# Kernel optimization log

Measured on AMD Instinct MI355X. Metric: run time of the kernel, lower is better.

The kernel has to match this reference:

```python
import jax, jax.numpy as jnp
import numpy as np

EPS = 1e-5

def conv2d(x, w, b=None, pad=0, groups=1):
    # x: NCHW, w: OIHW
    y = jax.lax.conv_general_dilated(
        x, w, window_strides=(1, 1), padding=[(pad, pad), (pad, pad)],
        dimension_numbers=('NCHW', 'OIHW', 'NCHW'), feature_group_count=groups)
    if b is not None:
        y = y + b[None, :, None, None]
    return y

def layernorm_c(x, w, b):
    # WithBias LayerNorm over channel dim of NCHW (matches to_3d -> LN(last dim=c) -> to_4d)
    mu = jnp.mean(x, axis=1, keepdims=True)
    var = jnp.mean((x - mu) ** 2, axis=1, keepdims=True)
    return (x - mu) / jnp.sqrt(var + EPS) * w[None, :, None, None] + b[None, :, None, None]

def setup_inputs() -> dict:
    key = jax.random.key(0)
    ks = iter(jax.random.split(key, 40))
    C, C8, Cc, Cs = 64, 8, 21, 2  # dim, dim//8, dim//compress_ratio, dim//squeeze_factor
    H = W = 64
    B = 4
    Hm = 128  # mlp hidden = dim * mlp_ratio
    s = 0.05
    def rn(shape):
        return jax.random.normal(next(ks), shape, dtype=jnp.float32) * s
    return {
        'x': jax.random.normal(next(ks), (B, C, H, W), dtype=jnp.float32),
        'ln_w': jnp.ones((C,), jnp.float32),
        'ln_b': jnp.zeros((C,), jnp.float32),
        'sab_q_w': rn((C8, C, 1, 1)), 'sab_q_b': rn((C8,)),
        'sab_k_w': rn((C8, C, 1, 1)), 'sab_k_b': rn((C8,)),
        'sab_v_w': rn((C, C, 1, 1)), 'sab_v_b': rn((C,)),
        'sab_qkdw_w': rn((C8, 1, 3, 3)), 'sab_qkdw_b': rn((C8,)),
        'sab_vdw_w': rn((C, 1, 3, 3)), 'sab_vdw_b': rn((C,)),
        'sab_proj_w': rn((C, C, 1, 1)), 'sab_proj_b': rn((C,)),
        'sab_gamma': jnp.zeros((1,), jnp.float32) + 0.1,
        'cab_w1': rn((Cc, C, 3, 3)), 'cab_b1': rn((Cc,)),
        'cab_w2': rn((C, Cc, 3, 3)), 'cab_b2': rn((C,)),
        'ca_w1': rn((Cs, C, 1, 1)), 'ca_b1': rn((Cs,)),
        'ca_w2': rn((C, Cs, 1, 1)), 'ca_b2': rn((C,)),
        'fc1_w': rn((Hm, C)), 'fc1_b': rn((Hm,)),
        'fc2_w': rn((C, Hm)), 'fc2_b': rn((C,)),
    }

def reference(x, ln_w, ln_b,
              sab_q_w, sab_q_b, sab_k_w, sab_k_b, sab_v_w, sab_v_b,
              sab_qkdw_w, sab_qkdw_b, sab_vdw_w, sab_vdw_b,
              sab_proj_w, sab_proj_b, sab_gamma,
              cab_w1, cab_b1, cab_w2, cab_b2,
              ca_w1, ca_b1, ca_w2, ca_b2,
              fc1_w, fc1_b, fc2_w, fc2_b):
    b, c, h, w = x.shape
    hw = h * w
    shortcut = x
    xn = layernorm_c(x, ln_w, ln_b)

    # --- SAB: full-pixel spatial self-attention ---
    C8 = sab_q_w.shape[0]
    q = conv2d(conv2d(xn, sab_q_w, sab_q_b), sab_qkdw_w, sab_qkdw_b, pad=1, groups=C8)
    k = conv2d(conv2d(xn, sab_k_w, sab_k_b), sab_qkdw_w, sab_qkdw_b, pad=1, groups=C8)
    v = conv2d(conv2d(xn, sab_v_w, sab_v_b), sab_vdw_w, sab_vdw_b, pad=1, groups=c)
    qf = q.reshape(b, C8, hw)          # (b, c8, n)
    kf = k.reshape(b, C8, hw)
    vf = v.reshape(b, c, hw)
    energy = jnp.einsum('bdi,bdj->bij', qf, kf)      # (b, hw, hw)
    attn = jax.nn.softmax(energy, axis=-1)
    out = jnp.einsum('bcj,bij->bci', vf, attn)        # (b, c, hw)
    out = out.reshape(b, c, h, w)
    out = conv2d(out, sab_proj_w, sab_proj_b)
    sa_feat = sab_gamma[0] * out + xn

    # --- CAB: conv compress/expand + RCAN channel attention ---
    y = conv2d(xn, cab_w1, cab_b1, pad=1)
    y = jax.nn.gelu(y, approximate=False)
    y = conv2d(y, cab_w2, cab_b2, pad=1)
    p = jnp.mean(y, axis=(2, 3), keepdims=True)       # adaptive avg pool to 1x1
    p = jax.nn.relu(conv2d(p, ca_w1, ca_b1))
    p = jax.nn.sigmoid(conv2d(p, ca_w2, ca_b2))
    ca_feat = y * p

    feat_sum = sa_feat + ca_feat + shortcut

    # --- MLP over channels (note: output is reshaped, NOT permuted back — faithful to source) ---
    fs1 = layernorm_c(feat_sum, ln_w, ln_b)
    t = fs1.transpose(0, 2, 3, 1).reshape(b, hw, c)   # (b, hw, c)
    t = jax.nn.gelu(t @ fc1_w.T + fc1_b, approximate=False)
    t = t @ fc2_w.T + fc2_b
    feat_sum2 = t.reshape(b, c, h, w)                 # raw view, matching torch .view(b,c,h,w)
    return feat_sum2 + feat_sum
```

## Files before the change

kernel.cpp:

```cpp
#include <hip/hip_runtime.h>
#include <math.h>

#define NB 4
#define NC 64
#define NC8 8
#define NCC 21
#define NHW 4096
#define NHM 128

typedef __attribute__((ext_vector_type(8))) short bf16x8;
typedef __attribute__((ext_vector_type(8))) unsigned short ushort8;
typedef __attribute__((ext_vector_type(4))) float f32x4;

__device__ __forceinline__ float gelu_exact(float x) {
    return 0.5f * x * (1.0f + erff(x * 0.70710678118654752f));
}

__device__ __forceinline__ unsigned short f2bf(float x) {
    union { float f; unsigned u; } u; u.f = x;
    unsigned r = u.u + 0x7fffu + ((u.u >> 16) & 1u);
    return (unsigned short)(r >> 16);
}

__device__ __forceinline__ float bf2f(unsigned short v) {
    union { unsigned u; float f; } t; t.u = (unsigned)v << 16; return t.f;
}

__global__ __launch_bounds__(256) void k_prep(const float* __restrict__ qw, const float* __restrict__ kw,
                     const float* __restrict__ vw, const float* __restrict__ c1w,
                     const float* __restrict__ c2w, const float* __restrict__ pw,
                     const float* __restrict__ f1w, const float* __restrict__ f2w,
                     float* __restrict__ o, float* __restrict__ pool,
                     const float* __restrict__ x, const float* __restrict__ lnw,
                     const float* __restrict__ lnb,
                     unsigned short* __restrict__ xn, unsigned short* __restrict__ xnT) {
    int bid = blockIdx.x;
    int tid = threadIdx.x;
    if (bid < 244) {
        int idx = bid * 256 + tid;
        if (idx < 256) pool[idx] = 0.f;
        if (idx < 5120) {
            int ci = idx / 80, j = idx - ci * 80;
            float v = j < 8 ? qw[j * 64 + ci] : (j < 16 ? kw[(j - 8) * 64 + ci] : vw[(j - 16) * 64 + ci]);
            o[idx] = v;
        } else if (idx < 9216) {
            int r = idx - 5120; int co = r & 63, ci = r >> 6;
            o[idx] = pw[co * 64 + ci];
        } else if (idx < 27648) {
            int r = idx - 9216;
            int j = r & 7, l = (r >> 3) & 63, s = (r >> 9) % 18, f = r / 9216;
            int co = f * 16 + (l & 15);
            int k = s * 32 + (l >> 4) * 8 + j;
            int tap = k >> 6, ci = k & 63;
            float v = (co < 21) ? c1w[co * 576 + ci * 9 + tap] : 0.f;
            unsigned short hi = f2bf(v);
            unsigned short lo = f2bf(v - bf2f(hi));
            ((unsigned short*)(o + 9216))[r] = hi;
            ((unsigned short*)(o + 18432))[r] = lo;
        } else if (idx < 46080) {
            int r = idx - 27648;
            int j = r & 7, l = (r >> 3) & 63, s = (r >> 9) % 9, f = r / 4608;
            int co = f * 16 + (l & 15);
            int ci = (l >> 4) * 8 + j;
            float v = (ci < 21) ? c2w[co * 189 + ci * 9 + s] : 0.f;
            unsigned short hi = f2bf(v);
            unsigned short lo = f2bf(v - bf2f(hi));
            ((unsigned short*)(o + 27648))[r] = hi;
            ((unsigned short*)(o + 36864))[r] = lo;
        } else if (idx < 54272) {
            int r = idx - 46080;
            int j = r & 7, l = (r >> 3) & 63, q = r >> 9;
            int F = q >> 1, s = q & 1;
            int m = F * 16 + (l & 15);
            int k = s * 32 + (l >> 4) * 8 + j;
            float v = f1w[m * 64 + k];
            unsigned short hi = f2bf(v);
            unsigned short lo = f2bf(v - bf2f(hi));
            ((unsigned short*)(o + 46080))[r] = hi;
            ((unsigned short*)(o + 50176))[r] = lo;
        } else if (idx < 62464) {
            int r = idx - 54272;
            int j = r & 7, l = (r >> 3) & 63, q = r >> 9;
            int F2 = q >> 2, s = q & 3;
            int wo = F2 * 16 + (l & 15);
            int k = s * 32 + (l >> 4) * 8 + j;
            float v = f2w[wo * 128 + k];
            unsigned short hi = f2bf(v);
            unsigned short lo = f2bf(v - bf2f(hi));
            ((unsigned short*)(o + 54272))[r] = hi;
            ((unsigned short*)(o + 58368))[r] = lo;
        }
        return;
    }
    __shared__ float r1[4][64], r2[4][64];
    int lb = bid - 244;
    int pl = tid & 63, cq = tid >> 6;
    int b = lb >> 6;
    int pix = (lb & 63) * 64 + pl;
    const float* p = x + (size_t)b * NC * NHW + pix;
    float v[16]; float s = 0.f, ss = 0.f;
    #pragma unroll
    for (int k = 0; k < 16; ++k) {
        float f = p[(size_t)(cq * 16 + k) * NHW];
        v[k] = f; s += f; ss += f * f;
    }
    r1[cq][pl] = s; r2[cq][pl] = ss;
    __syncthreads();
    float S  = r1[0][pl] + r1[1][pl] + r1[2][pl] + r1[3][pl];
    float SS = r2[0][pl] + r2[1][pl] + r2[2][pl] + r2[3][pl];
    float mean = S * (1.0f / 64);
    float rstd = rsqrtf(SS * (1.0f / 64) - mean * mean + 1e-5f);
    unsigned short* q = xn + (size_t)b * NC * NHW + pix;
    ushort8 t0, t1;
    #pragma unroll
    for (int k = 0; k < 16; ++k) {
        int c = cq * 16 + k;
        unsigned short bv = f2bf((v[k] - mean) * rstd * lnw[c] + lnb[c]);
        q[(size_t)c * NHW] = bv;
        if (k < 8) t0[k] = bv; else t1[k - 8] = bv;
    }
    unsigned short* tp = xnT + ((size_t)b * NHW + pix) * 64 + cq * 16;
    *(ushort8*)tp = t0;
    *(ushort8*)(tp + 8) = t1;
}

__global__ __launch_bounds__(512) void k_qkv(const unsigned short* __restrict__ xn,
        const float* __restrict__ wt, const float* __restrict__ qb,
        const float* __restrict__ kb, const float* __restrict__ vb,
        unsigned short* __restrict__ q1, unsigned short* __restrict__ k1,
        unsigned short* __restrict__ v1) {
    __shared__ unsigned short Xs[64][64];
    __shared__ float Ws[64][80];
    int tid = threadIdx.x;
    int pix0 = blockIdx.x * 64, b = blockIdx.y;
    for (int i = tid; i < 1024; i += 512) {
        int c = i >> 4, q4 = i & 15;
        *(ushort4*)&Xs[c][q4 * 4] = *(const ushort4*)(xn + ((size_t)b * NC + c) * NHW + pix0 + q4 * 4);
    }
    for (int i = tid; i < 1280; i += 512)
        *(float4*)&((float*)Ws)[i * 4] = *(const float4*)&wt[i * 4];
    __syncthreads();
    int p2 = (tid & 31) * 2, g = tid >> 5;
    int co0 = g * 5;
    float a0[5], a1[5];
    #pragma unroll
    for (int j = 0; j < 5; ++j) { a0[j] = 0.f; a1[j] = 0.f; }
    for (int ci = 0; ci < 64; ++ci) {
        ushort2 uv = *(const ushort2*)&Xs[ci][p2];
        float fx = bf2f(uv.x), fy = bf2f(uv.y);
        #pragma unroll
        for (int j = 0; j < 5; ++j) {
            float wv = Ws[ci][co0 + j];
            a0[j] = fmaf(fx, wv, a0[j]);
            a1[j] = fmaf(fy, wv, a1[j]);
        }
    }
    #pragma unroll
    for (int j = 0; j < 5; ++j) {
        int co = co0 + j;
        float bsv; unsigned short* dst;
        if (co < 8)       { bsv = qb[co];      dst = q1 + ((size_t)b * NC8 + co) * NHW + pix0 + p2; }
        else if (co < 16) { bsv = kb[co - 8];  dst = k1 + ((size_t)b * NC8 + co - 8) * NHW + pix0 + p2; }
        else              { bsv = vb[co - 16]; dst = v1 + ((size_t)b * NC + co - 16) * NHW + pix0 + p2; }
        ushort2 o = { f2bf(a0[j] + bsv), f2bf(a1[j] + bsv) };
        *(ushort2*)dst = o;
    }
}

__global__ __launch_bounds__(512) void k_dwcab1(
        const unsigned short* __restrict__ q1, const unsigned short* __restrict__ k1,
        const unsigned short* __restrict__ v1,
        const float* __restrict__ qkw, const float* __restrict__ qkb,
        const float* __restrict__ vw, const float* __restrict__ vb,
        unsigned short* __restrict__ qdb, unsigned short* __restrict__ kdb,
        unsigned short* __restrict__ v8,
        const unsigned short* __restrict__ xnT,
        const unsigned short* __restrict__ Ah, const unsigned short* __restrict__ Al,
        const float* __restrict__ bias, unsigned short* __restrict__ y1T) {
    __shared__ float Rs[2048];
    int bid = blockIdx.x;
    int tid = threadIdx.x;
    if (bid < 2560) {
        int pix = (bid & 7) * 512 + tid;
        int rest = bid >> 3;
        int yv = rest % 80, b = rest / 80;
        int y = pix >> 6, x = pix & 63;
        if (yv < 16) {
            int c = yv & 7;
            const unsigned short* ip = (yv < 8 ? q1 : k1) + ((size_t)b * NC8 + c) * NHW;
            const float* wp = qkw + c * 9;
            float acc = qkb[c];
            #pragma unroll
            for (int dy = -1; dy <= 1; ++dy) {
                int yy = y + dy; if (yy < 0 || yy > 63) continue;
                #pragma unroll
                for (int dx = -1; dx <= 1; ++dx) {
                    int xx = x + dx; if (xx < 0 || xx > 63) continue;
                    acc += wp[(dy + 1) * 3 + (dx + 1)] * bf2f(ip[yy * 64 + xx]);
                }
            }
            (yv < 8 ? qdb : kdb)[((size_t)b * NHW + pix) * NC8 + c] = f2bf(acc);
        } else {
            int c = yv - 16;
            const unsigned short* ip = v1 + ((size_t)b * NC + c) * NHW;
            const float* wp = vw + c * 9;
            float acc = vb[c];
            #pragma unroll
            for (int dy = -1; dy <= 1; ++dy) {
                int yy = y + dy; if (yy < 0 || yy > 63) continue;
                #pragma unroll
                for (int dx = -1; dx <= 1; ++dx) {
                    int xx = x + dx; if (xx < 0 || xx > 63) continue;
                    acc += wp[(dy + 1) * 3 + (dx + 1)] * bf2f(ip[yy * 64 + xx]);
                }
            }
            v8[(((size_t)b * 512 + (pix >> 3)) * NC + c) * 8 + (pix & 7)] = f2bf(acc);
        }
        return;
    }
    int r = bid - 2560;
    int y = r & 63, b = r >> 6;
    int w = tid >> 6, lane = tid & 63;
    int il = lane & 15, g = lane >> 4;
    int frag = w & 3, kh = w >> 2;
    int xloc = frag * 16 + il;
    f32x4 acc[2];
    acc[0] = (f32x4){0.f, 0.f, 0.f, 0.f};
    acc[1] = (f32x4){0.f, 0.f, 0.f, 0.f};
    #pragma unroll
    for (int si = 0; si < 9; ++si) {
        int s = kh * 9 + si;
        int tap = s >> 1;
        int ci0 = (s & 1) * 32;
        int dyv = tap / 3 - 1, dxv = tap - (tap / 3) * 3 - 1;
        int xx = xloc + dxv, yy = y + dyv;
        bf16x8 bv = (bf16x8)(short)0;
        if (((unsigned)xx < 64u) && ((unsigned)yy < 64u))
            bv = *(const bf16x8*)(xnT + ((size_t)b * NHW + yy * 64 + xx) * 64 + ci0 + g * 8);
        #pragma unroll
        for (int f = 0; f < 2; ++f) {
            bf16x8 ahv = *(const bf16x8*)(Ah + ((size_t)(f * 18 + s) * 64 + lane) * 8);
            bf16x8 alv = *(const bf16x8*)(Al + ((size_t)(f * 18 + s) * 64 + lane) * 8);
            acc[f] = __builtin_amdgcn_mfma_f32_16x16x32_bf16(ahv, bv, acc[f], 0, 0, 0);
            acc[f] = __builtin_amdgcn_mfma_f32_16x16x32_bf16(alv, bv, acc[f], 0, 0, 0);
        }
    }
    if (kh == 1) {
        #pragma unroll
        for (int f = 0; f < 2; ++f)
            #pragma unroll
            for (int e = 0; e < 4; ++e)
                Rs[((frag * 2 + f) * 4 + e) * 64 + lane] = acc[f][e];
    }
    __syncthreads();
    if (kh == 0) {
        #pragma unroll
        for (int f = 0; f < 2; ++f) {
            ushort4 pk;
            #pragma unroll
            for (int e = 0; e < 4; ++e) {
                float v = acc[f][e] + Rs[((frag * 2 + f) * 4 + e) * 64 + lane];
                int co = f * 16 + g * 4 + e;
                float rr = 0.f;
                if (co < 21) rr = gelu_exact(v + bias[co]);
                ((unsigned short*)&pk)[e] = f2bf(rr);
            }
            *(ushort4*)(y1T + ((size_t)b * NHW + y * 64 + xloc) * 32 + f * 16 + g * 4) = pk;
        }
    }
}

__global__ __launch_bounds__(512) void k_flashcab2(
        const unsigned short* __restrict__ qdb, const unsigned short* __restrict__ kdb,
        const unsigned short* __restrict__ v8, unsigned short* __restrict__ O,
        const unsigned short* __restrict__ y1T,
        const unsigned short* __restrict__ Ah, const unsigned short* __restrict__ Al,
        const float* __restrict__ bias, unsigned short* __restrict__ ycT,
        float* __restrict__ pool) {
    __shared__ __align__(16) char smem[35840];
    int bid = blockIdx.x;
    int tid = threadIdx.x;
    int w = tid >> 6, lane = tid & 63;
    int g = lane >> 4, il = lane & 15;
    if (bid < 512) {
        int i0 = (bid & 127) * 32, b = bid >> 7;
        unsigned short (*P)[72] = (unsigned short (*)[72])(smem + w * 2304);
        bf16x8 qb0 = (bf16x8)(short)0, qb1 = (bf16x8)(short)0;
        if (g == 0) {
            qb0 = *(const bf16x8*)(qdb + (size_t)(b * NHW + i0 + il) * NC8);
            qb1 = *(const bf16x8*)(qdb + (size_t)(b * NHW + i0 + 16 + il) * NC8);
        }
        f32x4 acc0[4], acc1[4];
        #pragma unroll
        for (int ct = 0; ct < 4; ++ct) {
            acc0[ct] = (f32x4){0.f, 0.f, 0.f, 0.f};
            acc1[ct] = (f32x4){0.f, 0.f, 0.f, 0.f};
        }
        float La0 = 0.f, La1 = 0.f;
        bf16x8 kn[4];
        #pragma unroll
        for (int t = 0; t < 4; ++t) {
            kn[t] = (bf16x8)(short)0;
            if (g == 0) kn[t] = *(const bf16x8*)(kdb + (size_t)(b * NHW + w * 512 + 16 * t + il) * NC8);
        }
        for (int jt = 0; jt < 8; ++jt) {
            int j0 = w * 512 + jt * 64;
            int ch0 = b * 512 + (j0 >> 3);
            bf16x8 va[2][4];
            #pragma unroll
            for (int kc = 0; kc < 2; ++kc)
                #pragma unroll
                for (int ct = 0; ct < 4; ++ct)
                    va[kc][ct] = *(const bf16x8*)(v8 +
                        ((size_t)(ch0 + kc * 4 + g) * NC + ct * 16 + il) * 8);
            bf16x8 ka[4];
            #pragma unroll
            for (int t = 0; t < 4; ++t) ka[t] = kn[t];
            if (jt < 7) {
                #pragma unroll
                for (int t = 0; t < 4; ++t) {
                    kn[t] = (bf16x8)(short)0;
                    if (g == 0) kn[t] = *(const bf16x8*)(kdb + (size_t)(b * NHW + j0 + 64 + 16 * t + il) * NC8);
                }
            }
            #pragma unroll
            for (int t = 0; t < 4; ++t) {
                f32x4 sv = __builtin_amdgcn_mfma_f32_16x16x32_bf16(ka[t], qb0, (f32x4){0.f, 0.f, 0.f, 0.f}, 0, 0, 0);
                float p0 = __expf(sv[0]), p1 = __expf(sv[1]);
                float p2 = __expf(sv[2]), p3 = __expf(sv[3]);
                La0 += (p0 + p1) + (p2 + p3);
                ushort4 pk;
                pk.x = f2bf(p0); pk.y = f2bf(p1); pk.z = f2bf(p2); pk.w = f2bf(p3);
                *(ushort4*)&P[il][16 * t + 4 * g] = pk;
            }
            #pragma unroll
            for (int kc = 0; kc < 2; ++kc) {
                bf16x8 pb = *(const bf16x8*)&P[il][kc * 32 + 8 * g];
                #pragma unroll
                for (int ct = 0; ct < 4; ++ct)
                    acc0[ct] = __builtin_amdgcn_mfma_f32_16x16x32_bf16(va[kc][ct], pb, acc0[ct], 0, 0, 0);
            }
            #pragma unroll
            for (int t = 0; t < 4; ++t) {
                f32x4 sv = __builtin_amdgcn_mfma_f32_16x16x32_bf16(ka[t], qb1, (f32x4){0.f, 0.f, 0.f, 0.f}, 0, 0, 0);
                float p0 = __expf(sv[0]), p1 = __expf(sv[1]);
                float p2 = __expf(sv[2]), p3 = __expf(sv[3]);
                La1 += (p0 + p1) + (p2 + p3);
                ushort4 pk;
                pk.x = f2bf(p0); pk.y = f2bf(p1); pk.z = f2bf(p2); pk.w = f2bf(p3);
                *(ushort4*)&P[il][16 * t + 4 * g] = pk;
            }
            #pragma unroll
            for (int kc = 0; kc < 2; ++kc) {
                bf16x8 pb = *(const bf16x8*)&P[il][kc * 32 + 8 * g];
                #pragma unroll
                for (int ct = 0; ct < 4; ++ct)
                    acc1[ct] = __builtin_amdgcn_mfma_f32_16x16x32_bf16(va[kc][ct], pb, acc1[ct], 0, 0, 0);
            }
        }
        La0 += __shfl_xor(La0, 16, 64); La0 += __shfl_xor(La0, 32, 64);
        La1 += __shfl_xor(La1, 16, 64); La1 += __shfl_xor(La1, 32, 64);

        __syncthreads();
        unsigned short* Ocm = (unsigned short*)smem;
        float* Lw = (float*)(smem + 34816);
        #pragma unroll
        for (int ct = 0; ct < 4; ++ct)
            #pragma unroll
            for (int e = 0; e < 4; ++e) {
                int c = ct * 16 + 4 * g + e;
                Ocm[(w * 2 + 0) * 1088 + c * 17 + il] = f2bf(acc0[ct][e]);
                Ocm[(w * 2 + 1) * 1088 + c * 17 + il] = f2bf(acc1[ct][e]);
            }
        if (lane < 16) {
            Lw[(w * 2 + 0) * 16 + il] = La0;
            Lw[(w * 2 + 1) * 16 + il] = La1;
        }
        __syncthreads();

        int st = tid >> 8, rem = tid & 255;
        int ic = rem & 15, ch = rem >> 4;
        float l = 0.f;
        #pragma unroll
        for (int w2 = 0; w2 < 8; ++w2) l += Lw[(w2 * 2 + st) * 16 + ic];
        float rl = 1.0f / l;
        #pragma unroll
        for (int cc = 0; cc < 4; ++cc) {
            int c = cc * 16 + ch;
            float o = 0.f;
            #pragma unroll
            for (int w2 = 0; w2 < 8; ++w2) o += bf2f(Ocm[(w2 * 2 + st) * 1088 + c * 17 + ic]);
            O[(size_t)(b * NC + c) * NHW + i0 + st * 16 + ic] = f2bf(o * rl);
        }
        return;
    }
    float* Rs = (float*)smem;
    float (*Ssum)[64] = (float (*)[64])(smem + 16384);
    int r = bid - 512;
    int y = r & 63, b = r >> 6;
    int frag = w & 3, kh = w >> 2;
    int xloc = frag * 16 + il;
    f32x4 acc[4];
    #pragma unroll
    for (int f = 0; f < 4; ++f) acc[f] = (f32x4){0.f, 0.f, 0.f, 0.f};
    #pragma unroll
    for (int si = 0; si < 5; ++si) {
        if (!(kh == 1 && si == 4)) {
            int s = kh * 5 + si;
            int dyv = s / 3 - 1, dxv = s - (s / 3) * 3 - 1;
            int xx = xloc + dxv, yy = y + dyv;
            bf16x8 bv = (bf16x8)(short)0;
            if (((unsigned)xx < 64u) && ((unsigned)yy < 64u))
                bv = *(const bf16x8*)(y1T + ((size_t)b * NHW + yy * 64 + xx) * 32 + g * 8);
            #pragma unroll
            for (int f = 0; f < 4; ++f) {
                bf16x8 ahv = *(const bf16x8*)(Ah + ((size_t)(f * 9 + s) * 64 + lane) * 8);
                bf16x8 alv = *(const bf16x8*)(Al + ((size_t)(f * 9 + s) * 64 + lane) * 8);
                acc[f] = __builtin_amdgcn_mfma_f32_16x16x32_bf16(ahv, bv, acc[f], 0, 0, 0);
                acc[f] = __builtin_amdgcn_mfma_f32_16x16x32_bf16(alv, bv, acc[f], 0, 0, 0);
            }
        }
    }
    if (kh == 1) {
        #pragma unroll
        for (int f = 0; f < 4; ++f)
            #pragma unroll
            for (int e = 0; e < 4; ++e)
                Rs[((frag * 4 + f) * 4 + e) * 64 + lane] = acc[f][e];
    }
    __syncthreads();
    if (kh == 0) {
        #pragma unroll
        for (int f = 0; f < 4; ++f) {
            ushort4 pk;
            #pragma unroll
            for (int e = 0; e < 4; ++e) {
                int co = f * 16 + g * 4 + e;
                float v = acc[f][e] + Rs[((frag * 4 + f) * 4 + e) * 64 + lane] + bias[co];
                ((unsigned short*)&pk)[e] = f2bf(v);
                float ps = v;
                ps += __shfl_xor(ps, 1, 64);
                ps += __shfl_xor(ps, 2, 64);
                ps += __shfl_xor(ps, 4, 64);
                ps += __shfl_xor(ps, 8, 64);
                if (il == 0) Ssum[frag][co] = ps;
            }
            *(ushort4*)(ycT + ((size_t)b * NHW + y * 64 + xloc) * 64 + f * 16 + g * 4) = pk;
        }
    }
    __syncthreads();
    if (tid < 64) {
        float t = Ssum[0][tid] + Ssum[1][tid] + Ssum[2][tid] + Ssum[3][tid];
        atomicAdd(&pool[b * NC + tid], t);
    }
}

__global__ __launch_bounds__(512) void k_fsum2(const unsigned short* __restrict__ O,
        const float* __restrict__ pwt, const float* __restrict__ pb,
        const float* __restrict__ gamma, const unsigned short* __restrict__ xnT,
        const unsigned short* __restrict__ ycT, const float* __restrict__ pool,
        const float* __restrict__ cw1, const float* __restrict__ cb1,
        const float* __restrict__ cw2, const float* __restrict__ cb2,
        const float* __restrict__ x, const float* __restrict__ lnw,
        const float* __restrict__ lnb, unsigned short* __restrict__ fsum,
        unsigned short* __restrict__ fs1T) {
    __shared__ unsigned short Os[64][64];
    __shared__ float Ws[64][64];
    __shared__ float Fs[64][66];
    __shared__ float mean_s[64], rstd_s[64];
    int tid = threadIdx.x;
    int pix0 = blockIdx.x * 64, b = blockIdx.y;
    for (int i = tid; i < 1024; i += 512) {
        int c = i >> 4, q4 = i & 15;
        *(ushort4*)&Os[c][q4 * 4] = *(const ushort4*)(O + ((size_t)b * NC + c) * NHW + pix0 + q4 * 4);
    }
    for (int i = tid; i < 1024; i += 512)
        *(float4*)&((float*)Ws)[i * 4] = *(const float4*)&pwt[i * 4];
    __syncthreads();
    float h0 = cb1[0], h1 = cb1[1];
    for (int ci = 0; ci < NC; ++ci) {
        float pv = pool[b * NC + ci] * (1.0f / NHW);
        h0 += cw1[ci] * pv;
        h1 += cw1[NC + ci] * pv;
    }
    h0 = fmaxf(h0, 0.f); h1 = fmaxf(h1, 0.f);
    int p2 = (tid & 31) * 2, g = tid >> 5;
    int co0 = g * 4;
    float scv[4];
    #pragma unroll
    for (int j = 0; j < 4; ++j) {
        int c = co0 + j;
        float z = cw2[c * 2] * h0 + cw2[c * 2 + 1] * h1 + cb2[c];
        scv[j] = 1.0f / (1.0f + __expf(-z));
    }
    float a0[4], a1[4];
    #pragma unroll
    for (int j = 0; j < 4; ++j) { a0[j] = 0.f; a1[j] = 0.f; }
    for (int ci = 0; ci < 64; ++ci) {
        ushort2 uv = *(const ushort2*)&Os[ci][p2];
        float ox = bf2f(uv.x), oy = bf2f(uv.y);
        float wv[4];
        *(float4*)wv = *(const float4*)&Ws[ci][co0];
        #pragma unroll
        for (int j = 0; j < 4; ++j) {
            a0[j] = fmaf(ox, wv[j], a0[j]);
            a1[j] = fmaf(oy, wv[j], a1[j]);
        }
    }
    float gg = gamma[0];
    size_t base = (size_t)b * NC * NHW + pix0 + p2;
    const unsigned short* xtp = xnT + ((size_t)b * NHW + pix0 + p2) * 64 + co0;
    const unsigned short* ytp = ycT + ((size_t)b * NHW + pix0 + p2) * 64 + co0;
    ushort4 xa = *(const ushort4*)xtp, xb = *(const ushort4*)(xtp + 64);
    ushort4 ya = *(const ushort4*)ytp, yb = *(const ushort4*)(ytp + 64);
    float f0[4], f1[4];
    #pragma unroll
    for (int j = 0; j < 4; ++j) {
        int c = co0 + j;
        size_t n = base + (size_t)c * NHW;
        float pbv = pb[c];
        float2 xv = *(const float2*)&x[n];
        f0[j] = gg * (a0[j] + pbv) + bf2f(((const unsigned short*)&xa)[j])
              + bf2f(((const unsigned short*)&ya)[j]) * scv[j] + xv.x;
        f1[j] = gg * (a1[j] + pbv) + bf2f(((const unsigned short*)&xb)[j])
              + bf2f(((const unsigned short*)&yb)[j]) * scv[j] + xv.y;
        ushort2 o = { f2bf(f0[j]), f2bf(f1[j]) };
        *(ushort2*)&fsum[n] = o;
        Fs[c][p2] = f0[j]; Fs[c][p2 + 1] = f1[j];
    }
    __syncthreads();
    if (tid < 64) {
        float s = 0.f, ss = 0.f;
        for (int c = 0; c < 64; ++c) { float v = Fs[c][tid]; s += v; ss += v * v; }
        float mean = s * (1.0f / 64);
        mean_s[tid] = mean;
        rstd_s[tid] = rsqrtf(ss * (1.0f / 64) - mean * mean + 1e-5f);
    }
    __syncthreads();
    float m0 = mean_s[p2], r0 = rstd_s[p2];
    float m1 = mean_s[p2 + 1], r1 = rstd_s[p2 + 1];
    ushort4 oA, oB;
    #pragma unroll
    for (int j = 0; j < 4; ++j) {
        int c = co0 + j;
        float lw = lnw[c], lb = lnb[c];
        ((unsigned short*)&oA)[j] = f2bf((f0[j] - m0) * r0 * lw + lb);
        ((unsigned short*)&oB)[j] = f2bf((f1[j] - m1) * r1 * lw + lb);
    }
    unsigned short* fp = fs1T + ((size_t)b * NHW + pix0 + p2) * 64 + co0;
    *(ushort4*)fp = oA;
    *(ushort4*)(fp + 64) = oB;
}

__global__ __launch_bounds__(512) void k_mlp(const unsigned short* __restrict__ fs1T,
        const unsigned short* __restrict__ A1h, const unsigned short* __restrict__ A1l,
        const float* __restrict__ b1,
        const unsigned short* __restrict__ A2h, const unsigned short* __restrict__ A2l,
        const float* __restrict__ b2,
        const unsigned short* __restrict__ fs, float* __restrict__ out) {
    __shared__ unsigned short Hs[64][136];
    int tid = threadIdx.x;
    int w = tid >> 6, lane = tid & 63;
    int il = lane & 15, g = lane >> 4;
    int frag = w & 3, fh = w >> 2;
    int y = blockIdx.x, b = blockIdx.y;
    int xloc = frag * 16 + il;
    const unsigned short* bp = fs1T + ((size_t)b * NHW + y * 64 + xloc) * 64;
    f32x4 acc[4];
    #pragma unroll
    for (int fi = 0; fi < 4; ++fi) acc[fi] = (f32x4){0.f, 0.f, 0.f, 0.f};
    #pragma unroll
    for (int s = 0; s < 2; ++s) {
        bf16x8 bv = *(const bf16x8*)(bp + s * 32 + g * 8);
        #pragma unroll
        for (int fi = 0; fi < 4; ++fi) {
            int F = fh * 4 + fi;
            bf16x8 ah = *(const bf16x8*)(A1h + ((size_t)(F * 2 + s) * 64 + lane) * 8);
            bf16x8 al = *(const bf16x8*)(A1l + ((size_t)(F * 2 + s) * 64 + lane) * 8);
            acc[fi] = __builtin_amdgcn_mfma_f32_16x16x32_bf16(ah, bv, acc[fi], 0, 0, 0);
            acc[fi] = __builtin_amdgcn_mfma_f32_16x16x32_bf16(al, bv, acc[fi], 0, 0, 0);
        }
    }
    #pragma unroll
    for (int fi = 0; fi < 4; ++fi) {
        int F = fh * 4 + fi;
        ushort4 pk;
        #pragma unroll
        for (int e = 0; e < 4; ++e) {
            int m = F * 16 + g * 4 + e;
            ((unsigned short*)&pk)[e] = f2bf(gelu_exact(acc[fi][e] + b1[m]));
        }
        *(ushort4*)&Hs[xloc][F * 16 + g * 4] = pk;
    }
    __syncthreads();
    f32x4 acc2[2];
    acc2[0] = (f32x4){0.f, 0.f, 0.f, 0.f};
    acc2[1] = (f32x4){0.f, 0.f, 0.f, 0.f};
    #pragma unroll
    for (int s = 0; s < 4; ++s) {
        bf16x8 bv = *(const bf16x8*)&Hs[xloc][s * 32 + g * 8];
        #pragma unroll
        for (int fi = 0; fi < 2; ++fi) {
            int F2 = fh * 2 + fi;
            bf16x8 ah = *(const bf16x8*)(A2h + ((size_t)(F2 * 4 + s) * 64 + lane) * 8);
            bf16x8 al = *(const bf16x8*)(A2l + ((size_t)(F2 * 4 + s) * 64 + lane) * 8);
            acc2[fi] = __builtin_amdgcn_mfma_f32_16x16x32_bf16(ah, bv, acc2[fi], 0, 0, 0);
            acc2[fi] = __builtin_amdgcn_mfma_f32_16x16x32_bf16(al, bv, acc2[fi], 0, 0, 0);
        }
    }
    #pragma unroll
    for (int fi = 0; fi < 2; ++fi) {
        int F2 = fh * 2 + fi;
        int c0 = F2 * 16 + g * 4;
        size_t ob = ((size_t)b * NHW + y * 64 + xloc) * 64 + c0;
        ushort4 rv = *(const ushort4*)&fs[ob];
        float4 o4;
        o4.x = acc2[fi][0] + b2[c0 + 0] + bf2f(rv.x);
        o4.y = acc2[fi][1] + b2[c0 + 1] + bf2f(rv.y);
        o4.z = acc2[fi][2] + b2[c0 + 2] + bf2f(rv.z);
        o4.w = acc2[fi][3] + b2[c0 + 3] + bf2f(rv.w);
        *(float4*)&out[ob] = o4;
    }
}

extern "C" void kernel_launch(void* const* d_in, const int* in_sizes, int n_in,
                              void* d_out, int out_size, void* d_ws, size_t ws_size,
                              hipStream_t stream) {
    const float* x        = (const float*)d_in[0];
    const float* ln_w     = (const float*)d_in[1];
    const float* ln_b     = (const float*)d_in[2];
    const float* q_w      = (const float*)d_in[3];
    const float* q_b      = (const float*)d_in[4];
    const float* k_w      = (const float*)d_in[5];
    const float* k_b      = (const float*)d_in[6];
    const float* v_w      = (const float*)d_in[7];
    const float* v_b      = (const float*)d_in[8];
    const float* qkdw_w   = (const float*)d_in[9];
    const float* qkdw_b   = (const float*)d_in[10];
    const float* vdw_w    = (const float*)d_in[11];
    const float* vdw_b    = (const float*)d_in[12];
    const float* proj_w   = (const float*)d_in[13];
    const float* proj_b   = (const float*)d_in[14];
    const float* gamma    = (const float*)d_in[15];
    const float* cab_w1   = (const float*)d_in[16];
    const float* cab_b1   = (const float*)d_in[17];
    const float* cab_w2   = (const float*)d_in[18];
    const float* cab_b2   = (const float*)d_in[19];
    const float* ca_w1    = (const float*)d_in[20];
    const float* ca_b1    = (const float*)d_in[21];
    const float* ca_w2    = (const float*)d_in[22];
    const float* ca_b2    = (const float*)d_in[23];
    const float* fc1_w    = (const float*)d_in[24];
    const float* fc1_b    = (const float*)d_in[25];
    const float* fc2_w    = (const float*)d_in[26];
    const float* fc2_b    = (const float*)d_in[27];
    float* out = (float*)d_out;

    char* ws = (char*)d_ws;
    size_t off = 0;
    auto alloc = [&](size_t bytes) { void* p = ws + off; off += (bytes + 255) & ~(size_t)255; return p; };
    unsigned short* xn  = (unsigned short*)alloc((size_t)NB * NC * NHW * 2);
    unsigned short* xnT = (unsigned short*)alloc((size_t)NB * NHW * NC * 2);
    unsigned short* q1  = (unsigned short*)alloc((size_t)NB * NC8 * NHW * 2);
    unsigned short* k1  = (unsigned short*)alloc((size_t)NB * NC8 * NHW * 2);
    unsigned short* v1  = (unsigned short*)alloc((size_t)NB * NC * NHW * 2);
    unsigned short* qdb = (unsigned short*)alloc((size_t)NB * NHW * NC8 * 2);
    unsigned short* kdb = (unsigned short*)alloc((size_t)NB * NHW * NC8 * 2);
    unsigned short* vdb = (unsigned short*)alloc((size_t)NB * NC * NHW * 2);
    unsigned short* O   = (unsigned short*)alloc((size_t)NB * NC * NHW * 2);
    unsigned short* y1T = (unsigned short*)alloc((size_t)NB * NHW * 32 * 2);
    unsigned short* ycT = (unsigned short*)alloc((size_t)NB * NHW * NC * 2);
    float* pool  = (float*)alloc(256 * 4);
    unsigned short* fsum = (unsigned short*)alloc((size_t)NB * NC * NHW * 2);
    unsigned short* fs1T = (unsigned short*)alloc((size_t)NB * NHW * NC * 2);
    float* wpack = (float*)alloc(62464 * 4);

    float* qkv_wt  = wpack;
    float* proj_wt = wpack + 5120;
    unsigned short* cab1Ah = (unsigned short*)(wpack + 9216);
    unsigned short* cab1Al = (unsigned short*)(wpack + 18432);
    unsigned short* cab2Ah = (unsigned short*)(wpack + 27648);
    unsigned short* cab2Al = (unsigned short*)(wpack + 36864);
    unsigned short* fc1h   = (unsigned short*)(wpack + 46080);
    unsigned short* fc1l   = (unsigned short*)(wpack + 50176);
    unsigned short* fc2h   = (unsigned short*)(wpack + 54272);
    unsigned short* fc2l   = (unsigned short*)(wpack + 58368);

    dim3 blk(256);
    dim3 blk5(512);

    k_prep<<<dim3(500), blk, 0, stream>>>(q_w, k_w, v_w, cab_w1, cab_w2, proj_w, fc1_w, fc2_w,
                                          wpack, pool, x, ln_w, ln_b, xn, xnT);
    k_qkv<<<dim3(64, NB), blk5, 0, stream>>>(xn, qkv_wt, q_b, k_b, v_b, q1, k1, v1);
    k_dwcab1<<<dim3(2816), blk5, 0, stream>>>(q1, k1, v1, qkdw_w, qkdw_b, vdw_w, vdw_b,
                                              qdb, kdb, vdb, xnT, cab1Ah, cab1Al, cab_b1, y1T);
    k_flashcab2<<<dim3(768), blk5, 0, stream>>>(qdb, kdb, vdb, O, y1T, cab2Ah, cab2Al,
                                                cab_b2, ycT, pool);
    k_fsum2<<<dim3(64, NB), blk5, 0, stream>>>(O, proj_wt, proj_b, gamma, xnT, ycT, pool,
                                               ca_w1, ca_b1, ca_w2, ca_b2, x, ln_w, ln_b,
                                               fsum, fs1T);
    k_mlp<<<dim3(64, NB), blk5, 0, stream>>>(fs1T, fc1h, fc1l, fc1_b, fc2h, fc2l, fc2_b,
                                             fsum, out);
}
```

Before: 190.7 us.

## Fuse QKV 1x1 projection into layernorm prep kernel, drop xn buffer

The separate k_qkv launch is removed. Its 1x1 conv is now computed inside the layernorm blocks of k_prep, using the normalized fp32 values kept in shared memory. This drops one kernel launch and the write and re-read of the channel-major bf16 xn buffer, and it skips the bf16 rounding on the QKV input. In exchange, each prep block loads the 80x64 weight slice from global memory with a strided gather, carries 20 accumulators per thread, and uses more shared memory, which may lower occupancy.

```diff
diff --git a/kernel.cpp b/kernel.cpp
--- a/kernel.cpp
+++ b/kernel.cpp
@@ -33,7 +33,11 @@
                      float* __restrict__ o, float* __restrict__ pool,
                      const float* __restrict__ x, const float* __restrict__ lnw,
                      const float* __restrict__ lnb,
-                     unsigned short* __restrict__ xn, unsigned short* __restrict__ xnT) {
+                     const float* __restrict__ qb, const float* __restrict__ kb,
+                     const float* __restrict__ vb,
+                     unsigned short* __restrict__ xnT,
+                     unsigned short* __restrict__ q1, unsigned short* __restrict__ k1,
+                     unsigned short* __restrict__ v1) {
     int bid = blockIdx.x;
     int tid = threadIdx.x;
     if (bid < 244) {
@@ -92,11 +96,19 @@
         }
         return;
     }
+    __shared__ float Xs[64][64];
+    __shared__ float Ws[64][80];
     __shared__ float r1[4][64], r2[4][64];
     int lb = bid - 244;
     int pl = tid & 63, cq = tid >> 6;
     int b = lb >> 6;
-    int pix = (lb & 63) * 64 + pl;
+    int pix0 = (lb & 63) * 64;
+    int pix = pix0 + pl;
+    for (int i = tid; i < 5120; i += 256) {
+        int ci = i / 80, j = i - ci * 80;
+        float v = j < 8 ? qw[j * 64 + ci] : (j < 16 ? kw[(j - 8) * 64 + ci] : vw[(j - 16) * 64 + ci]);
+        ((float*)Ws)[i] = v;
+    }
     const float* p = x + (size_t)b * NC * NHW + pix;
     float v[16]; float s = 0.f, ss = 0.f;
     #pragma unroll
@@ -110,60 +122,37 @@
     float SS = r2[0][pl] + r2[1][pl] + r2[2][pl] + r2[3][pl];
     float mean = S * (1.0f / 64);
     float rstd = rsqrtf(SS * (1.0f / 64) - mean * mean + 1e-5f);
-    unsigned short* q = xn + (size_t)b * NC * NHW + pix;
     ushort8 t0, t1;
     #pragma unroll
     for (int k = 0; k < 16; ++k) {
         int c = cq * 16 + k;
-        unsigned short bv = f2bf((v[k] - mean) * rstd * lnw[c] + lnb[c]);
-        q[(size_t)c * NHW] = bv;
+        float nv = (v[k] - mean) * rstd * lnw[c] + lnb[c];
+        Xs[c][pl] = nv;
+        unsigned short bv = f2bf(nv);
         if (k < 8) t0[k] = bv; else t1[k - 8] = bv;
     }
     unsigned short* tp = xnT + ((size_t)b * NHW + pix) * 64 + cq * 16;
     *(ushort8*)tp = t0;
     *(ushort8*)(tp + 8) = t1;
-}
-
-__global__ __launch_bounds__(512) void k_qkv(const unsigned short* __restrict__ xn,
-        const float* __restrict__ wt, const float* __restrict__ qb,
-        const float* __restrict__ kb, const float* __restrict__ vb,
-        unsigned short* __restrict__ q1, unsigned short* __restrict__ k1,
-        unsigned short* __restrict__ v1) {
-    __shared__ unsigned short Xs[64][64];
-    __shared__ float Ws[64][80];
-    int tid = threadIdx.x;
-    int pix0 = blockIdx.x * 64, b = blockIdx.y;
-    for (int i = tid; i < 1024; i += 512) {
-        int c = i >> 4, q4 = i & 15;
-        *(ushort4*)&Xs[c][q4 * 4] = *(const ushort4*)(xn + ((size_t)b * NC + c) * NHW + pix0 + q4 * 4);
-    }
-    for (int i = tid; i < 1280; i += 512)
-        *(float4*)&((float*)Ws)[i * 4] = *(const float4*)&wt[i * 4];
-    __syncthreads();
-    int p2 = (tid & 31) * 2, g = tid >> 5;
-    int co0 = g * 5;
-    float a0[5], a1[5];
-    #pragma unroll
-    for (int j = 0; j < 5; ++j) { a0[j] = 0.f; a1[j] = 0.f; }
+    __syncthreads();
+    int co0 = cq * 20;
+    float acc[20];
+    #pragma unroll
+    for (int j = 0; j < 20; ++j) acc[j] = 0.f;
     for (int ci = 0; ci < 64; ++ci) {
-        ushort2 uv = *(const ushort2*)&Xs[ci][p2];
-        float fx = bf2f(uv.x), fy = bf2f(uv.y);
-        #pragma unroll
-        for (int j = 0; j < 5; ++j) {
-            float wv = Ws[ci][co0 + j];
-            a0[j] = fmaf(fx, wv, a0[j]);
-            a1[j] = fmaf(fy, wv, a1[j]);
-        }
-    }
-    #pragma unroll
-    for (int j = 0; j < 5; ++j) {
+        float xv = Xs[ci][pl];
+        const float* wr = &Ws[ci][co0];
+        #pragma unroll
+        for (int j = 0; j < 20; ++j) acc[j] = fmaf(xv, wr[j], acc[j]);
+    }
+    #pragma unroll
+    for (int j = 0; j < 20; ++j) {
         int co = co0 + j;
         float bsv; unsigned short* dst;
-        if (co < 8)       { bsv = qb[co];      dst = q1 + ((size_t)b * NC8 + co) * NHW + pix0 + p2; }
-        else if (co < 16) { bsv = kb[co - 8];  dst = k1 + ((size_t)b * NC8 + co - 8) * NHW + pix0 + p2; }
-        else              { bsv = vb[co - 16]; dst = v1 + ((size_t)b * NC + co - 16) * NHW + pix0 + p2; }
-        ushort2 o = { f2bf(a0[j] + bsv), f2bf(a1[j] + bsv) };
-        *(ushort2*)dst = o;
+        if (co < 8)       { bsv = qb[co];      dst = q1 + ((size_t)b * NC8 + co) * NHW + pix; }
+        else if (co < 16) { bsv = kb[co - 8];  dst = k1 + ((size_t)b * NC8 + co - 8) * NHW + pix; }
+        else              { bsv = vb[co - 16]; dst = v1 + ((size_t)b * NC + co - 16) * NHW + pix; }
+        *dst = f2bf(acc[j] + bsv);
     }
 }
 
@@ -659,7 +648,6 @@
     char* ws = (char*)d_ws;
     size_t off = 0;
     auto alloc = [&](size_t bytes) { void* p = ws + off; off += (bytes + 255) & ~(size_t)255; return p; };
-    unsigned short* xn  = (unsigned short*)alloc((size_t)NB * NC * NHW * 2);
     unsigned short* xnT = (unsigned short*)alloc((size_t)NB * NHW * NC * 2);
     unsigned short* q1  = (unsigned short*)alloc((size_t)NB * NC8 * NHW * 2);
     unsigned short* k1  = (unsigned short*)alloc((size_t)NB * NC8 * NHW * 2);
@@ -675,7 +663,6 @@
     unsigned short* fs1T = (unsigned short*)alloc((size_t)NB * NHW * NC * 2);
     float* wpack = (float*)alloc(62464 * 4);
 
-    float* qkv_wt  = wpack;
     float* proj_wt = wpack + 5120;
     unsigned short* cab1Ah = (unsigned short*)(wpack + 9216);
     unsigned short* cab1Al = (unsigned short*)(wpack + 18432);
@@ -690,8 +677,8 @@
     dim3 blk5(512);
 
     k_prep<<<dim3(500), blk, 0, stream>>>(q_w, k_w, v_w, cab_w1, cab_w2, proj_w, fc1_w, fc2_w,
-                                          wpack, pool, x, ln_w, ln_b, xn, xnT);
-    k_qkv<<<dim3(64, NB), blk5, 0, stream>>>(xn, qkv_wt, q_b, k_b, v_b, q1, k1, v1);
+                                          wpack, pool, x, ln_w, ln_b, q_b, k_b, v_b,
+                                          xnT, q1, k1, v1);
     k_dwcab1<<<dim3(2816), blk5, 0, stream>>>(q1, k1, v1, qkdw_w, qkdw_b, vdw_w, vdw_b,
                                               qdb, kdb, vdb, xnT, cab1Ah, cab1Al, cab_b1, y1T);
     k_flashcab2<<<dim3(768), blk5, 0, stream>>>(qdb, kdb, vdb, O, y1T, cab2Ah, cab2Al,
```

After: 190.6 us. Within noise of the previous version (-0.0%).
